# Performance work log

Hardware: AMD Instinct MI355X
Metric: run time of the kernel (lower is better)

Reference implementation:

```python
import jax, jax.numpy as jnp
import numpy as np

TAU = 0.07        # temperature from init_kwargs
EPS = 1e-8        # torch F.cosine_similarity eps
NEG_INF = -1e9    # mask fill value used by the original module


def setup_inputs() -> dict:
    key = jax.random.key(0)
    k1, k2 = jax.random.split(key)
    B, D = 4096, 512
    anchor = jax.random.normal(k1, (B, D), dtype=jnp.float32)
    positive = jax.random.normal(k2, (B, D), dtype=jnp.float32)
    return {"anchor": anchor, "positive": positive}


def reference(anchor, positive):
    B = anchor.shape[0]
    N = 2 * B
    emb = jnp.concatenate([anchor, positive], axis=0)          # (2B, D)
    # cosine similarity matrix == normalized dot products (same math as the
    # broadcasted F.cosine_similarity, without the O(N^2 D) intermediate)
    norm = jnp.maximum(jnp.linalg.norm(emb, axis=1, keepdims=True), EPS)
    z = emb / norm
    sim = jnp.matmul(z, z.T) / TAU                             # (2B, 2B)

    idx = jnp.arange(N)
    pos_idx = (idx + B) % N                                    # positive pair index
    pos_logits = sim[idx, pos_idx][:, None]                    # (2B, 1)

    # negatives: everything except self and the positive pair
    neg_mask = (
        jnp.ones((N, N), dtype=bool)
        .at[idx, idx].set(False)
        .at[idx, pos_idx].set(False)
    )
    neg_logits = jnp.where(neg_mask, sim, NEG_INF)             # (2B, 2B)

    all_logits = jnp.concatenate([pos_logits, neg_logits], axis=1)  # (2B, 2B+1)
    loss_per_sample = -pos_logits[:, 0] + jax.scipy.special.logsumexp(all_logits, axis=1)
    # every row has a positive, so valid_samples is all-True; reduction='mean'
    return loss_per_sample.mean()
```

## Files before the change

### kernel.cpp

```cpp
#include <hip/hip_runtime.h>
#include <hip/hip_bf16.h>
#include <stdint.h>


#define N_TOT   8192
#define B_HALF  4096
#define DDIM    512
#define INV_TAU 14.285714285714286f
#define TTILES  32
#define NKT     16

typedef __bf16 bf16x8 __attribute__((ext_vector_type(8)));
typedef __bf16 bf16x4 __attribute__((ext_vector_type(4)));
typedef float  floatx4 __attribute__((ext_vector_type(4)));

__device__ __forceinline__ void gl2lds16(const void* g, void* l) {
    __builtin_amdgcn_global_load_lds(
        (const __attribute__((address_space(1))) void*)g,
        (__attribute__((address_space(3))) void*)l, 16, 0, 0);
}

#define S_BARRIER() asm volatile("s_barrier" ::: "memory")
#define LGKM0()     do { asm volatile("s_waitcnt lgkmcnt(0)" ::: "memory"); \
                         __builtin_amdgcn_sched_barrier(0); } while (0)
#define VMCNT4()    asm volatile("s_waitcnt vmcnt(4)" ::: "memory")
#define VMCNT0()    asm volatile("s_waitcnt vmcnt(0)" ::: "memory")
#define VM_NONE()   do {} while (0)

__global__ __launch_bounds__(256) void knorm(const float* __restrict__ anchor,
                                             const float* __restrict__ positive,
                                             __bf16* __restrict__ z,
                                             float* __restrict__ row_sums) {
    const int row  = blockIdx.x * 4 + (threadIdx.x >> 6);
    const int lane = threadIdx.x & 63;
    if (lane == 0) row_sums[row] = 0.0f;
    const float* src = (row < B_HALF) ? (anchor + (size_t)row * DDIM)
                                      : (positive + (size_t)(row - B_HALF) * DDIM);
    float4 v0 = ((const float4*)src)[lane];
    float4 v1 = ((const float4*)src)[lane + 64];
    float ss = v0.x*v0.x + v0.y*v0.y + v0.z*v0.z + v0.w*v0.w
             + v1.x*v1.x + v1.y*v1.y + v1.z*v1.z + v1.w*v1.w;
    #pragma unroll
    for (int m = 1; m < 64; m <<= 1) ss += __shfl_xor(ss, m, 64);
    const float inv = 1.0f / fmaxf(sqrtf(ss), 1e-8f);
    bf16x4 o0, o1;
    o0[0] = (__bf16)(v0.x*inv); o0[1] = (__bf16)(v0.y*inv);
    o0[2] = (__bf16)(v0.z*inv); o0[3] = (__bf16)(v0.w*inv);
    o1[0] = (__bf16)(v1.x*inv); o1[1] = (__bf16)(v1.y*inv);
    o1[2] = (__bf16)(v1.z*inv); o1[3] = (__bf16)(v1.w*inv);
    bf16x4* dst = (bf16x4*)(z + (size_t)row * DDIM);
    dst[lane]      = o0;
    dst[lane + 64] = o1;
}

__global__ __launch_bounds__(512, 2) void ksim(const __bf16* __restrict__ z,
                                               float* __restrict__ row_sums,
                                               float* __restrict__ pos_sims) {
    int bid = (int)blockIdx.x;
    bid = (bid & 7) * 66 + (bid >> 3);
    int rem = bid, rt = 0;
    while (rem >= TTILES - rt) { rem -= TTILES - rt; rt++; }
    const int ct = rt + rem;
    const bool diag = (rt == ct);
    const bool posb = (ct == rt + 16);

    const int r0 = rt * 256, c0 = ct * 256;
    const int tid  = threadIdx.x;
    const int w    = tid >> 6, lane = tid & 63;
    const int quad = lane >> 4, nlo = lane & 15;
    const int wr   = w >> 2,   wc  = w & 3;

    __shared__ __align__(16) char smem[4][32768];

    const __bf16* zA = z + (size_t)(r0 + w * 16 + (lane >> 2)) * DDIM + (lane & 3) * 8;
    const __bf16* zB = z + (size_t)(c0 + w * 16 + (lane >> 2)) * DDIM + (lane & 3) * 8;

#define STAGE_A(T2) do { char* s_ = smem[(T2) & 3]; const int kb_ = (T2) * 32;   \
        gl2lds16(zA + kb_,              s_ + w * 1024);                          \
        gl2lds16(zA + 128 * DDIM + kb_, s_ + 8192 + w * 1024); } while (0)
#define STAGE_B(T2) do { char* s_ = smem[(T2) & 3]; const int kb_ = (T2) * 32;   \
        gl2lds16(zB + kb_,              s_ + 16384 + w * 1024);                  \
        gl2lds16(zB + 128 * DDIM + kb_, s_ + 16384 + 8192 + w * 1024); } while (0)

    floatx4 acc[8][4];
    #pragma unroll
    for (int a = 0; a < 8; a++)
        #pragma unroll
        for (int b = 0; b < 4; b++) acc[a][b] = (floatx4){0.f, 0.f, 0.f, 0.f};

    STAGE_A(0); STAGE_B(0);
    STAGE_A(1); STAGE_B(1);
    VMCNT4();
    S_BARRIER();

#define KTILE(T, DO_STAGE, VMW) do {                                                  \
        char* As_ = smem[(T) & 3];                                                    \
        char* Bs_ = As_ + 16384;                                                      \
        bf16x8 af[4], bfr[4];                                                         \
                                                    \
        _Pragma("unroll") for (int mi = 0; mi < 4; mi++)                              \
            af[mi] = *(const bf16x8*)(As_ + (wr * 128 + mi * 16 + nlo) * 64 + quad * 16); \
        _Pragma("unroll") for (int ni = 0; ni < 4; ni++)                              \
            bfr[ni] = *(const bf16x8*)(Bs_ + (wc * 64 + ni * 16 + nlo) * 64 + quad * 16); \
        if (DO_STAGE) STAGE_A((T) + 2);                                               \
        S_BARRIER(); LGKM0();                                                         \
        __builtin_amdgcn_s_setprio(1);                                                \
        _Pragma("unroll") for (int mi = 0; mi < 4; mi++)                              \
            _Pragma("unroll") for (int ni = 0; ni < 4; ni++)                          \
                acc[mi][ni] = __builtin_amdgcn_mfma_f32_16x16x32_bf16(                \
                    af[mi], bfr[ni], acc[mi][ni], 0, 0, 0);                           \
        __builtin_amdgcn_s_setprio(0);                                                \
        S_BARRIER();                                                                  \
                           \
        _Pragma("unroll") for (int mi = 0; mi < 4; mi++)                              \
            af[mi] = *(const bf16x8*)(As_ + (wr * 128 + 64 + mi * 16 + nlo) * 64 + quad * 16); \
        if (DO_STAGE) STAGE_B((T) + 2);                                               \
        S_BARRIER(); LGKM0();                                                         \
        __builtin_amdgcn_s_setprio(1);                                                \
        _Pragma("unroll") for (int mi = 0; mi < 4; mi++)                              \
            _Pragma("unroll") for (int ni = 0; ni < 4; ni++)                          \
                acc[4 + mi][ni] = __builtin_amdgcn_mfma_f32_16x16x32_bf16(            \
                    af[mi], bfr[ni], acc[4 + mi][ni], 0, 0, 0);                       \
        __builtin_amdgcn_s_setprio(0);                                                \
        VMW();                                                                        \
        S_BARRIER();                                                                  \
    } while (0)

    for (int t = 0; t < NKT - 2; ++t) KTILE(t, true, VMCNT4);
    KTILE(NKT - 2, false, VMCNT0);
    KTILE(NKT - 1, false, VM_NONE);

    __syncthreads();
    float* rbuf = (float*)smem;
    float* cbuf = (float*)(smem[0] + 4096);

    float cs[4] = {0.f, 0.f, 0.f, 0.f};
    #pragma unroll
    for (int mi = 0; mi < 8; mi++) {
        #pragma unroll
        for (int reg = 0; reg < 4; reg++) {
            const int il = wr * 128 + mi * 16 + quad * 4 + reg;
            const int i  = r0 + il;
            const int ipos = i ^ B_HALF;
            float rs = 0.f;
            #pragma unroll
            for (int ni = 0; ni < 4; ni++) {
                const int j = c0 + wc * 64 + ni * 16 + nlo;
                const float sim = acc[mi][ni][reg] * INV_TAU;
                float e = __expf(sim - INV_TAU);
                if (diag && j == i) e = 0.f;
                if (posb && j == ipos) {
                    pos_sims[i] = sim;
                    pos_sims[j] = sim;
                }
                rs += e;
                cs[ni] += e;
            }
            rs += __shfl_xor(rs, 1, 64);
            rs += __shfl_xor(rs, 2, 64);
            rs += __shfl_xor(rs, 4, 64);
            rs += __shfl_xor(rs, 8, 64);
            if (nlo == 0) rbuf[il * 4 + wc] = rs;
        }
    }
    if (!diag) {
        #pragma unroll
        for (int ni = 0; ni < 4; ni++) {
            float c = cs[ni];
            c += __shfl_xor(c, 16, 64);
            c += __shfl_xor(c, 32, 64);
            if (quad == 0) cbuf[(wc * 64 + ni * 16 + nlo) * 2 + wr] = c;
        }
    }
    __syncthreads();
    if (tid < 256) {
        const float s = rbuf[tid * 4] + rbuf[tid * 4 + 1]
                      + rbuf[tid * 4 + 2] + rbuf[tid * 4 + 3];
        atomicAdd(&row_sums[r0 + tid], s);
    } else if (!diag) {
        const int c = tid - 256;
        atomicAdd(&row_sums[c0 + c], cbuf[c * 2] + cbuf[c * 2 + 1]);
    }
#undef KTILE
#undef STAGE_A
#undef STAGE_B
}

__global__ __launch_bounds__(1024) void kfinal(const float* __restrict__ row_sums,
                                               const float* __restrict__ pos_sims,
                                               float* __restrict__ out) {
    const int tid = threadIdx.x;
    float acc = 0.f;
    for (int i = tid; i < N_TOT; i += 1024)
        acc += INV_TAU + __logf(row_sums[i]) - pos_sims[i];
    #pragma unroll
    for (int m = 1; m < 64; m <<= 1) acc += __shfl_xor(acc, m, 64);
    __shared__ float wsum[16];
    if ((tid & 63) == 0) wsum[tid >> 6] = acc;
    __syncthreads();
    if (tid < 16) {
        float v = wsum[tid];
        #pragma unroll
        for (int m = 1; m < 16; m <<= 1) v += __shfl_xor(v, m, 64);
        if (tid == 0) out[0] = v / (float)N_TOT;
    }
}

extern "C" void kernel_launch(void* const* d_in, const int* in_sizes, int n_in,
                              void* d_out, int out_size, void* d_ws, size_t ws_size,
                              hipStream_t stream) {
    const float* anchor   = (const float*)d_in[0];
    const float* positive = (const float*)d_in[1];
    float* out = (float*)d_out;

    char* ws = (char*)d_ws;
    __bf16* z        = (__bf16*)ws;
    float*  row_sums = (float*)(ws + 8388608);
    float*  pos_sims = (float*)(ws + 8388608 + 32768);

    knorm<<<N_TOT / 4, 256, 0, stream>>>(anchor, positive, z, row_sums);
    ksim<<<528, 512, 0, stream>>>(z, row_sums, pos_sims);
    kfinal<<<1, 1024, 0, stream>>>(row_sums, pos_sims, out);
}
```

Baseline: 138.6 us.

## Swizzle LDS tile layout to avoid bank conflicts and parallelize final reduction

Applies an XOR swizzle to the 16-byte chunk index when staging z tiles into LDS and when reading MFMA fragments, so lanes in a quad group hit different LDS banks. Separately, it replaces the single-block final reduction with 32 blocks that each atomically add a partial mean into the output, which is zeroed in the normalization kernel. The swizzle aims to remove LDS bank conflicts in the matmul inner loop. The atomic reduction makes the result order-dependent in float rounding.

```diff
diff --git a/kernel.cpp b/kernel.cpp
--- a/kernel.cpp
+++ b/kernel.cpp
@@ -30,10 +30,12 @@
 __global__ __launch_bounds__(256) void knorm(const float* __restrict__ anchor,
                                              const float* __restrict__ positive,
                                              __bf16* __restrict__ z,
-                                             float* __restrict__ row_sums) {
+                                             float* __restrict__ row_sums,
+                                             float* __restrict__ out) {
     const int row  = blockIdx.x * 4 + (threadIdx.x >> 6);
     const int lane = threadIdx.x & 63;
     if (lane == 0) row_sums[row] = 0.0f;
+    if (blockIdx.x == 0 && threadIdx.x == 0) out[0] = 0.0f;
     const float* src = (row < B_HALF) ? (anchor + (size_t)row * DDIM)
                                       : (positive + (size_t)(row - B_HALF) * DDIM);
     float4 v0 = ((const float4*)src)[lane];
@@ -69,11 +71,13 @@
     const int w    = tid >> 6, lane = tid & 63;
     const int quad = lane >> 4, nlo = lane & 15;
     const int wr   = w >> 2,   wc  = w & 3;
+    const int s4   = (nlo >> 1) & 3;
 
     __shared__ __align__(16) char smem[4][32768];
 
-    const __bf16* zA = z + (size_t)(r0 + w * 16 + (lane >> 2)) * DDIM + (lane & 3) * 8;
-    const __bf16* zB = z + (size_t)(c0 + w * 16 + (lane >> 2)) * DDIM + (lane & 3) * 8;
+    const int schunk = ((lane & 3) ^ ((lane >> 3) & 3)) * 8;
+    const __bf16* zA = z + (size_t)(r0 + w * 16 + (lane >> 2)) * DDIM + schunk;
+    const __bf16* zB = z + (size_t)(c0 + w * 16 + (lane >> 2)) * DDIM + schunk;
 
 #define STAGE_A(T2) do { char* s_ = smem[(T2) & 3]; const int kb_ = (T2) * 32;   \
         gl2lds16(zA + kb_,              s_ + w * 1024);                          \
@@ -99,9 +103,11 @@
         bf16x8 af[4], bfr[4];                                                         \
                                                     \
         _Pragma("unroll") for (int mi = 0; mi < 4; mi++)                              \
-            af[mi] = *(const bf16x8*)(As_ + (wr * 128 + mi * 16 + nlo) * 64 + quad * 16); \
+            af[mi] = *(const bf16x8*)(As_ + (wr * 128 + mi * 16 + nlo) * 64           \
+                                          + ((quad ^ s4) * 16));                      \
         _Pragma("unroll") for (int ni = 0; ni < 4; ni++)                              \
-            bfr[ni] = *(const bf16x8*)(Bs_ + (wc * 64 + ni * 16 + nlo) * 64 + quad * 16); \
+            bfr[ni] = *(const bf16x8*)(Bs_ + (wc * 64 + ni * 16 + nlo) * 64           \
+                                           + ((quad ^ s4) * 16));                     \
         if (DO_STAGE) STAGE_A((T) + 2);                                               \
         S_BARRIER(); LGKM0();                                                         \
         __builtin_amdgcn_s_setprio(1);                                                \
@@ -113,7 +119,8 @@
         S_BARRIER();                                                                  \
                            \
         _Pragma("unroll") for (int mi = 0; mi < 4; mi++)                              \
-            af[mi] = *(const bf16x8*)(As_ + (wr * 128 + 64 + mi * 16 + nlo) * 64 + quad * 16); \
+            af[mi] = *(const bf16x8*)(As_ + (wr * 128 + 64 + mi * 16 + nlo) * 64      \
+                                          + ((quad ^ s4) * 16));                      \
         if (DO_STAGE) STAGE_B((T) + 2);                                               \
         S_BARRIER(); LGKM0();                                                         \
         __builtin_amdgcn_s_setprio(1);                                                \
@@ -186,24 +193,18 @@
 #undef STAGE_B
 }
 
-__global__ __launch_bounds__(1024) void kfinal(const float* __restrict__ row_sums,
-                                               const float* __restrict__ pos_sims,
-                                               float* __restrict__ out) {
-    const int tid = threadIdx.x;
-    float acc = 0.f;
-    for (int i = tid; i < N_TOT; i += 1024)
-        acc += INV_TAU + __logf(row_sums[i]) - pos_sims[i];
-    #pragma unroll
-    for (int m = 1; m < 64; m <<= 1) acc += __shfl_xor(acc, m, 64);
-    __shared__ float wsum[16];
-    if ((tid & 63) == 0) wsum[tid >> 6] = acc;
+__global__ __launch_bounds__(256) void kfinal(const float* __restrict__ row_sums,
+                                              const float* __restrict__ pos_sims,
+                                              float* __restrict__ out) {
+    const int r = blockIdx.x * 256 + threadIdx.x;
+    float v = INV_TAU + __logf(row_sums[r]) - pos_sims[r];
+    #pragma unroll
+    for (int m = 1; m < 64; m <<= 1) v += __shfl_xor(v, m, 64);
+    __shared__ float wsum[4];
+    if ((threadIdx.x & 63) == 0) wsum[threadIdx.x >> 6] = v;
     __syncthreads();
-    if (tid < 16) {
-        float v = wsum[tid];
-        #pragma unroll
-        for (int m = 1; m < 16; m <<= 1) v += __shfl_xor(v, m, 64);
-        if (tid == 0) out[0] = v / (float)N_TOT;
-    }
+    if (threadIdx.x == 0)
+        atomicAdd(out, (wsum[0] + wsum[1] + wsum[2] + wsum[3]) * (1.0f / (float)N_TOT));
 }
 
 extern "C" void kernel_launch(void* const* d_in, const int* in_sizes, int n_in,
@@ -218,7 +219,7 @@
     float*  row_sums = (float*)(ws + 8388608);
     float*  pos_sims = (float*)(ws + 8388608 + 32768);
 
-    knorm<<<N_TOT / 4, 256, 0, stream>>>(anchor, positive, z, row_sums);
+    knorm<<<N_TOT / 4, 256, 0, stream>>>(anchor, positive, z, row_sums, out);
     ksim<<<528, 512, 0, stream>>>(z, row_sums, pos_sims);
-    kfinal<<<1, 1024, 0, stream>>>(row_sums, pos_sims, out);
-}
+    kfinal<<<N_TOT / 256, 256, 0, stream>>>(row_sums, pos_sims, out);
+}
```

After: 137.5 us. Within noise of the previous version (-0.8%).
